# Kernel optimization log

Measured on AMD Instinct MI355X. Metric: run time of the kernel, lower is better.

The kernel has to match this reference:

```python
import jax, jax.numpy as jnp
import numpy as np


def setup_inputs() -> dict:
    key = jax.random.key(0)
    ks = jax.random.split(key, 11)
    N, K, M = 2, 2048, 1024   # batch, seq_len, d_model (dim_in)
    H, D = 16, 64             # num_heads, dim_out (per-head q/k/v dim)
    s_in = 1.0 / np.sqrt(M)
    s_out = 1.0 / np.sqrt(H * D)
    return {
        "query": jax.random.normal(ks[0], (N, K, M), jnp.float32),
        "key":   jax.random.normal(ks[1], (N, K, M), jnp.float32),
        "value": jax.random.normal(ks[2], (N, K, M), jnp.float32),
        "Wq": jax.random.normal(ks[3], (H, D, M), jnp.float32) * s_in,
        "bq": jax.random.normal(ks[4], (H, D), jnp.float32) * 0.01,
        "Wk": jax.random.normal(ks[5], (H, D, M), jnp.float32) * s_in,
        "bk": jax.random.normal(ks[6], (H, D), jnp.float32) * 0.01,
        "Wv": jax.random.normal(ks[7], (H, D, M), jnp.float32) * s_in,
        "bv": jax.random.normal(ks[8], (H, D), jnp.float32) * 0.01,
        "Wo": jax.random.normal(ks[9], (M, H * D), jnp.float32) * s_out,
        "bo": jax.random.normal(ks[10], (M,), jnp.float32) * 0.01,
    }


def reference(query, key, value, Wq, bq, Wk, bk, Wv, bv, Wo, bo):
    # Batched over heads instead of the original python loop; same math.
    # q,k: [H,N,K,D], v: [H,N,K,D]
    q = jnp.einsum('nkm,hdm->hnkd', query, Wq) + bq[:, None, None, :]
    k = jnp.einsum('nkm,hdm->hnkd', key,   Wk) + bk[:, None, None, :]
    v = jnp.einsum('nkm,hdm->hnkd', value, Wv) + bv[:, None, None, :]
    D = q.shape[-1]
    # scaled_dot_product scales by sqrt of the projected dim (dim_out)
    scores = jnp.einsum('hnkd,hnld->hnkl', q, k) / jnp.sqrt(jnp.asarray(D, q.dtype))
    attn = jax.nn.softmax(scores, axis=-1)            # [H,N,K,K]
    y = jnp.einsum('hnkl,hnld->hnkd', attn, v)        # [H,N,K,D]
    H, N, K, _ = y.shape
    # concat heads along feature dim: [N,K,H*D]
    y_cat = jnp.transpose(y, (1, 2, 0, 3)).reshape(N, K, H * D)
    return y_cat @ Wo.T + bo
```

## Files before the change

### kernel.cpp

```cpp
#include <hip/hip_runtime.h>
#include <hip/hip_bf16.h>

#define NB 2
#define SEQ 2048
#define DM 1024
#define NH 16
#define HD 64

typedef unsigned short u16;
typedef unsigned int u32;
typedef __attribute__((ext_vector_type(8))) short bf16x8;
typedef __attribute__((ext_vector_type(4))) float f32x4;
typedef __attribute__((ext_vector_type(4))) unsigned short u16x4;
typedef __attribute__((ext_vector_type(2))) unsigned int u32x2;

#define MFMA __builtin_amdgcn_mfma_f32_16x16x32_bf16

#define QSCALE 0.18033688011112042f

__device__ __forceinline__ u16 bf16_rne(float x) {
    unsigned int u = __float_as_uint(x);
    return (u16)((u + 0x7FFFu + ((u >> 16) & 1u)) >> 16);
}
__device__ __forceinline__ float bf16f(u16 h) {
    return __uint_as_float(((unsigned int)h) << 16);
}
__device__ __forceinline__ void split2(float x, u16& h, u16& l) {
    h = bf16_rne(x);
    l = bf16_rne(x - bf16f(h));
}
__device__ __forceinline__ u32 cvt_pk_bf16(float lo, float hi) {
    u32 r;
    asm("v_cvt_pk_bf16_f32 %0, %1, %2" : "=v"(r) : "v"(lo), "v"(hi));
    return r;
}
__device__ __forceinline__ float exp2_fast(float x) {
#if __has_builtin(__builtin_amdgcn_exp2f)
    return __builtin_amdgcn_exp2f(x);
#else
    float r;
    asm("v_exp_f32 %0, %1" : "=v"(r) : "v"(x));
    return r;
#endif
}

__device__ __forceinline__ void async16(const u16* g, u16* l) {
    typedef const __attribute__((address_space(1))) u32* GP;
    typedef __attribute__((address_space(3))) u32* LP;
    __builtin_amdgcn_global_load_lds((GP)g, (LP)l, 16, 0, 0);
}

__global__ __launch_bounds__(256) void presplit(
    const float* __restrict__ x0, const float* __restrict__ x1,
    const float* __restrict__ x2, const float* __restrict__ wq,
    const float* __restrict__ wk, const float* __restrict__ wv,
    const float* __restrict__ wo,
    u16* __restrict__ xh, u16* __restrict__ xl,
    u16* __restrict__ wh, u16* __restrict__ wl)
{
    const int seg = blockIdx.y;
    const float* src;
    u16 *dh, *dl;
    int n4;
    float sc = 1.f;
    if (seg < 3) {
        src = (seg == 0) ? x0 : (seg == 1) ? x1 : x2;
        dh = xh + (size_t)seg * 4194304;
        dl = xl + (size_t)seg * 4194304;
        n4 = 1048576;
    } else {
        int s2 = seg - 3;
        src = (s2 == 0) ? wq : (s2 == 1) ? wk : (s2 == 2) ? wv : wo;
        dh = wh + (size_t)s2 * 1048576;
        dl = wl + (size_t)s2 * 1048576;
        n4 = 262144;
        if (s2 == 0) sc = QSCALE;
    }
    for (int i = blockIdx.x * 256 + threadIdx.x; i < n4; i += gridDim.x * 256) {
        float4 v = ((const float4*)src)[i];
        u16 h0, h1, h2, h3, l0, l1, l2, l3;
        split2(v.x * sc, h0, l0); split2(v.y * sc, h1, l1);
        split2(v.z * sc, h2, l2); split2(v.w * sc, h3, l3);
        u16x4 hv = {h0, h1, h2, h3}, lv = {l0, l1, l2, l3};
        *(u16x4*)(dh + (size_t)i * 4) = hv;
        *(u16x4*)(dl + (size_t)i * 4) = lv;
    }
}

template<int VAR>
__global__ __launch_bounds__(256, 2) void gemm2(
    const u16* __restrict__ xh3, const u16* __restrict__ xl3,
    const u16* __restrict__ wh4, const u16* __restrict__ wl4,
    const float* bq, const float* bk, const float* bv,
    u16* qh, u16* ql, u16* kh, u16* kl, u16* vh, u16* vl,
    float* outf)
{
    __shared__ u16 Ah[128][32], Al[128][32], Bh[128][32], Bl[128][32];

    const int tid = threadIdx.x, lane = tid & 63, w = tid >> 6;
    const int lg = lane >> 4, lc = lane & 15;

    const int id = blockIdx.x + 8 * blockIdx.y;
    const int swz = (id & 7) * 32 + (id >> 3);
    const int c0 = (swz & 7) * 128, r0 = (swz >> 3) * 128;

    const u16 *ag, *alg, *bg, *blg;
    const float* bias;
    u16 *oh = nullptr, *ol = nullptr;
    float bsc = 1.f;
    int mode;
    if (VAR == 0) {
        const int z = blockIdx.z;
        ag  = xh3 + (size_t)z * 4194304;
        alg = xl3 + (size_t)z * 4194304;
        bg  = wh4 + (size_t)z * 1048576;
        blg = wl4 + (size_t)z * 1048576;
        if (z == 0)      { bias = bq; oh = qh; ol = ql; bsc = QSCALE; mode = 1; }
        else if (z == 1) { bias = bk; oh = kh; mode = 2; }
        else             { bias = bv; oh = vh; mode = 3; }
    } else {
        ag = xh3; alg = xl3; bg = wh4; blg = wl4; bias = bq; mode = 0;
    }

    const u16* gb = (w == 0) ? ag : (w == 1) ? alg : (w == 2) ? bg : blg;
    u16* lb = (w == 0) ? &Ah[0][0] : (w == 1) ? &Al[0][0] : (w == 2) ? &Bh[0][0] : &Bl[0][0];
    const int rbase = (w < 2) ? r0 : c0;
    const u16* gsrc0 = gb + (size_t)(rbase + (lane >> 2)) * DM + (lane & 3) * 8;

    const int wr = (w >> 1) * 64, wc = (w & 1) * 64;

    f32x4 acc[4][4];
#pragma unroll
    for (int i = 0; i < 4; ++i)
#pragma unroll
        for (int j = 0; j < 4; ++j) acc[i][j] = (f32x4)0.f;

    for (int ks = 0; ks < DM; ks += 32) {
        __syncthreads();
#pragma unroll
        for (int i = 0; i < 8; ++i)
            async16(gsrc0 + (size_t)i * 16 * DM + ks, lb + i * 512);
        __syncthreads();

        bf16x8 ah[4], al[4];
#pragma unroll
        for (int rt = 0; rt < 4; ++rt) {
            ah[rt] = *(const bf16x8*)&Ah[wr + rt * 16 + lc][lg * 8];
            al[rt] = *(const bf16x8*)&Al[wr + rt * 16 + lc][lg * 8];
        }
#pragma unroll
        for (int jt = 0; jt < 4; ++jt) {
            bf16x8 bh2 = *(const bf16x8*)&Bh[wc + jt * 16 + lc][lg * 8];
            bf16x8 bl2 = *(const bf16x8*)&Bl[wc + jt * 16 + lc][lg * 8];
#pragma unroll
            for (int rt = 0; rt < 4; ++rt) {
                acc[rt][jt] = MFMA(ah[rt], bh2, acc[rt][jt], 0, 0, 0);
                acc[rt][jt] = MFMA(ah[rt], bl2, acc[rt][jt], 0, 0, 0);
                acc[rt][jt] = MFMA(al[rt], bh2, acc[rt][jt], 0, 0, 0);
            }
        }
    }

#pragma unroll
    for (int rt = 0; rt < 4; ++rt)
#pragma unroll
        for (int jt = 0; jt < 4; ++jt)
#pragma unroll
            for (int r = 0; r < 4; ++r) {
                int row = r0 + wr + rt * 16 + lg * 4 + r;
                int col = c0 + wc + jt * 16 + lc;
                float v = acc[rt][jt][r] + bias[col] * bsc;
                if (mode == 0) {
                    outf[(size_t)row * DM + col] = v;
                } else {
                    int h = col >> 6, d = col & 63, n = row >> 11, s = row & 2047;
                    if (mode == 1) {
                        size_t idx = ((size_t)((h << 1) | n) * SEQ + s) * HD + d;
                        u16 hh, ll; split2(v, hh, ll);
                        oh[idx] = hh; ol[idx] = ll;
                    } else if (mode == 2) {
                        size_t idx = ((size_t)((h << 1) | n) * SEQ + s) * HD + d;
                        oh[idx] = bf16_rne(v);
                    } else {
                        size_t idx = ((size_t)((h << 1) | n) * HD + d) * SEQ + s;
                        oh[idx] = bf16_rne(v);
                    }
                }
            }
}

__global__ __launch_bounds__(256, 4) void attn_k(
    const u16* __restrict__ qh, const u16* __restrict__ ql,
    const u16* __restrict__ kh, const u16* __restrict__ vth,
    u16* __restrict__ yh, u16* __restrict__ yl)
{
    __shared__ u16 Ks[64][72], Vs[64][72];
    __shared__ u16 Pb[4][32][72];

    const int tid = threadIdx.x, lane = tid & 63, w = tid >> 6;
    const int lg = lane >> 4, lc = lane & 15;

    const int id = blockIdx.x + 16 * blockIdx.y;
    const int widx = (id & 7) * 64 + (id >> 3);
    const int hn = widx >> 4;
    const int qb0 = (widx & 15) * 128;

    bf16x8 qfh[2][2], qfl[2][2];
    const size_t qkbase = (size_t)hn * SEQ * HD;
#pragma unroll
    for (int rt = 0; rt < 2; ++rt)
#pragma unroll
        for (int kc = 0; kc < 2; ++kc) {
            size_t off = qkbase + (size_t)(qb0 + w * 32 + rt * 16 + lc) * HD + kc * 32 + lg * 8;
            qfh[rt][kc] = *(const bf16x8*)(qh + off);
            qfl[rt][kc] = *(const bf16x8*)(ql + off);
        }

    f32x4 ot[2][4];
#pragma unroll
    for (int i = 0; i < 2; ++i)
#pragma unroll
        for (int j = 0; j < 4; ++j) ot[i][j] = (f32x4)0.f;
    float m_[2] = {-3e38f, -3e38f};
    float s_[2] = {0.f, 0.f};

    const size_t vbase = (size_t)hn * HD * SEQ;

    for (int kt = 0; kt < SEQ; kt += 64) {
        __syncthreads();
#pragma unroll
        for (int i = 0; i < 2; ++i) {
            int f = tid + 256 * i, row = f >> 3, kb = (f & 7) * 8;
            size_t ksrc = qkbase + (size_t)(kt + row) * HD + kb;
            *(bf16x8*)&Ks[row][kb] = *(const bf16x8*)(kh + ksrc);
            size_t vsrc = vbase + (size_t)row * SEQ + kt + kb;
            *(bf16x8*)&Vs[row][kb] = *(const bf16x8*)(vth + vsrc);
        }
        __syncthreads();

        f32x4 st[2][4];
#pragma unroll
        for (int i = 0; i < 2; ++i)
#pragma unroll
            for (int j = 0; j < 4; ++j) st[i][j] = (f32x4)0.f;
        __builtin_amdgcn_s_setprio(1);
#pragma unroll
        for (int jt = 0; jt < 4; ++jt)
#pragma unroll
            for (int kc = 0; kc < 2; ++kc) {
                bf16x8 k8 = *(const bf16x8*)&Ks[jt * 16 + lc][kc * 32 + lg * 8];
#pragma unroll
                for (int rt = 0; rt < 2; ++rt) {
                    st[rt][jt] = MFMA(k8, qfh[rt][kc], st[rt][jt], 0, 0, 0);
                    st[rt][jt] = MFMA(k8, qfl[rt][kc], st[rt][jt], 0, 0, 0);
                }
            }
        __builtin_amdgcn_s_setprio(0);

#pragma unroll
        for (int rt = 0; rt < 2; ++rt) {
            float t0 = fmaxf(fmaxf(st[rt][0][0], st[rt][0][1]),
                             fmaxf(st[rt][0][2], st[rt][0][3]));
            float t1 = fmaxf(fmaxf(st[rt][1][0], st[rt][1][1]),
                             fmaxf(st[rt][1][2], st[rt][1][3]));
            float t2 = fmaxf(fmaxf(st[rt][2][0], st[rt][2][1]),
                             fmaxf(st[rt][2][2], st[rt][2][3]));
            float t3 = fmaxf(fmaxf(st[rt][3][0], st[rt][3][1]),
                             fmaxf(st[rt][3][2], st[rt][3][3]));
            float t = fmaxf(fmaxf(t0, t1), fmaxf(t2, t3));
            t = fmaxf(t, __shfl_xor(t, 16));
            t = fmaxf(t, __shfl_xor(t, 32));
            if (__any(t - m_[rt] > 8.0f)) {
                float mnew = fmaxf(m_[rt], t);
                float resc = exp2_fast(m_[rt] - mnew);
                m_[rt] = mnew;
                s_[rt] *= resc;
#pragma unroll
                for (int dt = 0; dt < 4; ++dt) {
                    ot[rt][dt][0] *= resc; ot[rt][dt][1] *= resc;
                    ot[rt][dt][2] *= resc; ot[rt][dt][3] *= resc;
                }
            }
            const float mm = m_[rt];
#pragma unroll
            for (int jt = 0; jt < 4; ++jt) {
                float p0 = exp2_fast(st[rt][jt][0] - mm);
                float p1 = exp2_fast(st[rt][jt][1] - mm);
                float p2 = exp2_fast(st[rt][jt][2] - mm);
                float p3 = exp2_fast(st[rt][jt][3] - mm);
                s_[rt] += (p0 + p1) + (p2 + p3);
                u32x2 pk = {cvt_pk_bf16(p0, p1), cvt_pk_bf16(p2, p3)};
                *(u32x2*)&Pb[w][rt * 16 + lc][jt * 16 + lg * 4] = pk;
            }
        }

        bf16x8 pb[2][2];
#pragma unroll
        for (int rt = 0; rt < 2; ++rt)
#pragma unroll
            for (int jc = 0; jc < 2; ++jc)
                pb[rt][jc] = *(const bf16x8*)&Pb[w][rt * 16 + lc][jc * 32 + lg * 8];
        __builtin_amdgcn_s_setprio(1);
#pragma unroll
        for (int dt = 0; dt < 4; ++dt)
#pragma unroll
            for (int jc = 0; jc < 2; ++jc) {
                bf16x8 v8 = *(const bf16x8*)&Vs[dt * 16 + lc][jc * 32 + lg * 8];
#pragma unroll
                for (int rt = 0; rt < 2; ++rt)
                    ot[rt][dt] = MFMA(v8, pb[rt][jc], ot[rt][dt], 0, 0, 0);
            }
        __builtin_amdgcn_s_setprio(0);
    }

    const int h = hn >> 1, n = hn & 1;
#pragma unroll
    for (int rt = 0; rt < 2; ++rt) {
        float v = s_[rt];
        v += __shfl_xor(v, 16);
        v += __shfl_xor(v, 32);
        s_[rt] = 1.f / v;
    }
#pragma unroll
    for (int rt = 0; rt < 2; ++rt) {
        const int srow = qb0 + w * 32 + rt * 16 + lc;
        size_t rowoff = (size_t)(n * SEQ + srow) * DM + h * HD;
#pragma unroll
        for (int dt = 0; dt < 4; ++dt) {
            u16x4 hv, lv;
#pragma unroll
            for (int r = 0; r < 4; ++r) {
                float y = ot[rt][dt][r] * s_[rt];
                u16 hh, ll; split2(y, hh, ll);
                hv[r] = hh; lv[r] = ll;
            }
            size_t idx = rowoff + dt * 16 + lg * 4;
            *(u16x4*)(yh + idx) = hv;
            *(u16x4*)(yl + idx) = lv;
        }
    }
}

extern "C" void kernel_launch(void* const* d_in, const int* in_sizes, int n_in,
                              void* d_out, int out_size, void* d_ws, size_t ws_size,
                              hipStream_t stream)
{
    const float* query = (const float*)d_in[0];
    const float* key_  = (const float*)d_in[1];
    const float* value = (const float*)d_in[2];
    const float* Wq = (const float*)d_in[3];
    const float* bq = (const float*)d_in[4];
    const float* Wk = (const float*)d_in[5];
    const float* bk = (const float*)d_in[6];
    const float* Wv = (const float*)d_in[7];
    const float* bv = (const float*)d_in[8];
    const float* Wo = (const float*)d_in[9];
    const float* bo = (const float*)d_in[10];
    float* out = (float*)d_out;

    char* p = (char*)d_ws;
    u16* wh  = (u16*)(p);
    u16* wl  = (u16*)(p + 8388608ull);
    u16* qh  = (u16*)(p + 16777216ull);
    u16* ql  = (u16*)(p + 25165824ull);
    u16* kh  = (u16*)(p + 33554432ull);
    u16* kl  = (u16*)(p + 41943040ull);
    u16* vth = (u16*)(p + 50331648ull);
    u16* vtl = (u16*)(p + 58720256ull);
    u16* xh  = (u16*)(p + 67108864ull);
    u16* xl  = (u16*)(p + 92274688ull);
    u16* yh  = (u16*)(p + 67108864ull);
    u16* yl  = (u16*)(p + 75497472ull);

    presplit<<<dim3(256, 7), 256, 0, stream>>>(
        query, key_, value, Wq, Wk, Wv, Wo, xh, xl, wh, wl);

    gemm2<0><<<dim3(8, 32, 3), 256, 0, stream>>>(
        xh, xl, wh, wl, bq, bk, bv,
        qh, ql, kh, kl, vth, vtl, nullptr);

    attn_k<<<dim3(16, 32), 256, 0, stream>>>(qh, ql, kh, vth, yh, yl);

    gemm2<1><<<dim3(8, 32, 1), 256, 0, stream>>>(
        yh, yl, wh + 3145728ull, wl + 3145728ull, bo, nullptr, nullptr,
        nullptr, nullptr, nullptr, nullptr, nullptr, nullptr, out);
}
```

Baseline: 332.3 us.

## Drop low-bf16 split for QKV projections and use single-pass bf16 GEMM

```diff
diff --git a/kernel.cpp b/kernel.cpp
--- a/kernel.cpp
+++ b/kernel.cpp
@@ -55,47 +55,48 @@
     const float* __restrict__ x2, const float* __restrict__ wq,
     const float* __restrict__ wk, const float* __restrict__ wv,
     const float* __restrict__ wo,
-    u16* __restrict__ xh, u16* __restrict__ xl,
-    u16* __restrict__ wh, u16* __restrict__ wl)
+    u16* __restrict__ xh, u16* __restrict__ wh, u16* __restrict__ wl)
 {
     const int seg = blockIdx.y;
     const float* src;
-    u16 *dh, *dl;
+    u16* dh;
+    u16* dl = nullptr;
     int n4;
     float sc = 1.f;
     if (seg < 3) {
         src = (seg == 0) ? x0 : (seg == 1) ? x1 : x2;
         dh = xh + (size_t)seg * 4194304;
-        dl = xl + (size_t)seg * 4194304;
         n4 = 1048576;
     } else {
         int s2 = seg - 3;
         src = (s2 == 0) ? wq : (s2 == 1) ? wk : (s2 == 2) ? wv : wo;
         dh = wh + (size_t)s2 * 1048576;
-        dl = wl + (size_t)s2 * 1048576;
+        if (s2 == 3) dl = wl + (size_t)s2 * 1048576;
         n4 = 262144;
         if (s2 == 0) sc = QSCALE;
     }
     for (int i = blockIdx.x * 256 + threadIdx.x; i < n4; i += gridDim.x * 256) {
         float4 v = ((const float4*)src)[i];
-        u16 h0, h1, h2, h3, l0, l1, l2, l3;
-        split2(v.x * sc, h0, l0); split2(v.y * sc, h1, l1);
-        split2(v.z * sc, h2, l2); split2(v.w * sc, h3, l3);
-        u16x4 hv = {h0, h1, h2, h3}, lv = {l0, l1, l2, l3};
+        v.x *= sc; v.y *= sc; v.z *= sc; v.w *= sc;
+        u16 h0 = bf16_rne(v.x), h1 = bf16_rne(v.y);
+        u16 h2 = bf16_rne(v.z), h3 = bf16_rne(v.w);
+        u16x4 hv = {h0, h1, h2, h3};
         *(u16x4*)(dh + (size_t)i * 4) = hv;
-        *(u16x4*)(dl + (size_t)i * 4) = lv;
-    }
-}
-
-template<int VAR>
-__global__ __launch_bounds__(256, 2) void gemm2(
-    const u16* __restrict__ xh3, const u16* __restrict__ xl3,
-    const u16* __restrict__ wh4, const u16* __restrict__ wl4,
-    const float* bq, const float* bk, const float* bv,
-    u16* qh, u16* ql, u16* kh, u16* kl, u16* vh, u16* vl,
-    float* outf)
+        if (dl) {
+            u16x4 lv = {bf16_rne(v.x - bf16f(h0)), bf16_rne(v.y - bf16f(h1)),
+                        bf16_rne(v.z - bf16f(h2)), bf16_rne(v.w - bf16f(h3))};
+            *(u16x4*)(dl + (size_t)i * 4) = lv;
+        }
+    }
+}
+
+__global__ __launch_bounds__(256, 4) void gemm_qkv(
+    const u16* __restrict__ xh3, const u16* __restrict__ wh3,
+    const float* __restrict__ bq, const float* __restrict__ bk,
+    const float* __restrict__ bv,
+    u16* qh, u16* ql, u16* kh, u16* vth)
 {
-    __shared__ u16 Ah[128][32], Al[128][32], Bh[128][32], Bl[128][32];
+    __shared__ u16 A0[128][32], A1[128][32], B0[128][32], B1[128][32];
 
     const int tid = threadIdx.x, lane = tid & 63, w = tid >> 6;
     const int lg = lane >> 4, lc = lane & 15;
@@ -104,25 +105,93 @@
     const int swz = (id & 7) * 32 + (id >> 3);
     const int c0 = (swz & 7) * 128, r0 = (swz >> 3) * 128;
 
-    const u16 *ag, *alg, *bg, *blg;
-    const float* bias;
-    u16 *oh = nullptr, *ol = nullptr;
-    float bsc = 1.f;
-    int mode;
-    if (VAR == 0) {
-        const int z = blockIdx.z;
-        ag  = xh3 + (size_t)z * 4194304;
-        alg = xl3 + (size_t)z * 4194304;
-        bg  = wh4 + (size_t)z * 1048576;
-        blg = wl4 + (size_t)z * 1048576;
-        if (z == 0)      { bias = bq; oh = qh; ol = ql; bsc = QSCALE; mode = 1; }
-        else if (z == 1) { bias = bk; oh = kh; mode = 2; }
-        else             { bias = bv; oh = vh; mode = 3; }
-    } else {
-        ag = xh3; alg = xl3; bg = wh4; blg = wl4; bias = bq; mode = 0;
-    }
-
-    const u16* gb = (w == 0) ? ag : (w == 1) ? alg : (w == 2) ? bg : blg;
+    const int z = blockIdx.z;
+    const u16* ag = xh3 + (size_t)z * 4194304;
+    const u16* bg = wh3 + (size_t)z * 1048576;
+    const float* bias = (z == 0) ? bq : (z == 1) ? bk : bv;
+
+    const u16* gb = (w < 2) ? ag : bg;
+    u16* lb = (w == 0) ? &A0[0][0] : (w == 1) ? &A1[0][0]
+            : (w == 2) ? &B0[0][0] : &B1[0][0];
+    const int rbase = (w < 2) ? r0 : c0;
+    const int colofs = (w & 1) * 32;
+    const u16* gsrc0 = gb + (size_t)(rbase + (lane >> 2)) * DM + colofs + (lane & 3) * 8;
+
+    const int wr = (w >> 1) * 64, wc = (w & 1) * 64;
+
+    f32x4 acc[4][4];
+#pragma unroll
+    for (int i = 0; i < 4; ++i)
+#pragma unroll
+        for (int j = 0; j < 4; ++j) acc[i][j] = (f32x4)0.f;
+
+    for (int ks = 0; ks < DM; ks += 64) {
+        __syncthreads();
+#pragma unroll
+        for (int i = 0; i < 8; ++i)
+            async16(gsrc0 + (size_t)i * 16 * DM + ks, lb + i * 512);
+        __syncthreads();
+
+#pragma unroll
+        for (int kk = 0; kk < 2; ++kk) {
+            const u16(*Ak)[32] = kk ? A1 : A0;
+            const u16(*Bk)[32] = kk ? B1 : B0;
+            bf16x8 ah[4], bh[4];
+#pragma unroll
+            for (int rt = 0; rt < 4; ++rt)
+                ah[rt] = *(const bf16x8*)&Ak[wr + rt * 16 + lc][lg * 8];
+#pragma unroll
+            for (int jt = 0; jt < 4; ++jt)
+                bh[jt] = *(const bf16x8*)&Bk[wc + jt * 16 + lc][lg * 8];
+#pragma unroll
+            for (int jt = 0; jt < 4; ++jt)
+#pragma unroll
+                for (int rt = 0; rt < 4; ++rt)
+                    acc[rt][jt] = MFMA(ah[rt], bh[jt], acc[rt][jt], 0, 0, 0);
+        }
+    }
+
+#pragma unroll
+    for (int rt = 0; rt < 4; ++rt)
+#pragma unroll
+        for (int jt = 0; jt < 4; ++jt)
+#pragma unroll
+            for (int r = 0; r < 4; ++r) {
+                int row = r0 + wr + rt * 16 + lg * 4 + r;
+                int col = c0 + wc + jt * 16 + lc;
+                int h = col >> 6, d = col & 63, n = row >> 11, s = row & 2047;
+                if (z == 0) {
+                    float v = acc[rt][jt][r] + bias[col] * QSCALE;
+                    size_t idx = ((size_t)((h << 1) | n) * SEQ + s) * HD + d;
+                    u16 hh, ll; split2(v, hh, ll);
+                    qh[idx] = hh; ql[idx] = ll;
+                } else if (z == 1) {
+                    float v = acc[rt][jt][r] + bias[col];
+                    size_t idx = ((size_t)((h << 1) | n) * SEQ + s) * HD + d;
+                    kh[idx] = bf16_rne(v);
+                } else {
+                    float v = acc[rt][jt][r] + bias[col];
+                    size_t idx = ((size_t)((h << 1) | n) * HD + d) * SEQ + s;
+                    vth[idx] = bf16_rne(v);
+                }
+            }
+}
+
+__global__ __launch_bounds__(256, 2) void gemm_proj(
+    const u16* __restrict__ yh, const u16* __restrict__ yl,
+    const u16* __restrict__ woh, const u16* __restrict__ wol,
+    const float* __restrict__ bo, float* __restrict__ outf)
+{
+    __shared__ u16 Ah[128][32], Al[128][32], Bh[128][32], Bl[128][32];
+
+    const int tid = threadIdx.x, lane = tid & 63, w = tid >> 6;
+    const int lg = lane >> 4, lc = lane & 15;
+
+    const int id = blockIdx.x + 8 * blockIdx.y;
+    const int swz = (id & 7) * 32 + (id >> 3);
+    const int c0 = (swz & 7) * 128, r0 = (swz >> 3) * 128;
+
+    const u16* gb = (w == 0) ? yh : (w == 1) ? yl : (w == 2) ? woh : wol;
     u16* lb = (w == 0) ? &Ah[0][0] : (w == 1) ? &Al[0][0] : (w == 2) ? &Bh[0][0] : &Bl[0][0];
     const int rbase = (w < 2) ? r0 : c0;
     const u16* gsrc0 = gb + (size_t)(rbase + (lane >> 2)) * DM + (lane & 3) * 8;
@@ -169,23 +238,7 @@
             for (int r = 0; r < 4; ++r) {
                 int row = r0 + wr + rt * 16 + lg * 4 + r;
                 int col = c0 + wc + jt * 16 + lc;
-                float v = acc[rt][jt][r] + bias[col] * bsc;
-                if (mode == 0) {
-                    outf[(size_t)row * DM + col] = v;
-                } else {
-                    int h = col >> 6, d = col & 63, n = row >> 11, s = row & 2047;
-                    if (mode == 1) {
-                        size_t idx = ((size_t)((h << 1) | n) * SEQ + s) * HD + d;
-                        u16 hh, ll; split2(v, hh, ll);
-                        oh[idx] = hh; ol[idx] = ll;
-                    } else if (mode == 2) {
-                        size_t idx = ((size_t)((h << 1) | n) * SEQ + s) * HD + d;
-                        oh[idx] = bf16_rne(v);
-                    } else {
-                        size_t idx = ((size_t)((h << 1) | n) * HD + d) * SEQ + s;
-                        oh[idx] = bf16_rne(v);
-                    }
-                }
+                outf[(size_t)row * DM + col] = acc[rt][jt][r] + bo[col];
             }
 }
 
@@ -364,24 +417,19 @@
     u16* qh  = (u16*)(p + 16777216ull);
     u16* ql  = (u16*)(p + 25165824ull);
     u16* kh  = (u16*)(p + 33554432ull);
-    u16* kl  = (u16*)(p + 41943040ull);
     u16* vth = (u16*)(p + 50331648ull);
-    u16* vtl = (u16*)(p + 58720256ull);
     u16* xh  = (u16*)(p + 67108864ull);
-    u16* xl  = (u16*)(p + 92274688ull);
     u16* yh  = (u16*)(p + 67108864ull);
     u16* yl  = (u16*)(p + 75497472ull);
 
     presplit<<<dim3(256, 7), 256, 0, stream>>>(
-        query, key_, value, Wq, Wk, Wv, Wo, xh, xl, wh, wl);
-
-    gemm2<0><<<dim3(8, 32, 3), 256, 0, stream>>>(
-        xh, xl, wh, wl, bq, bk, bv,
-        qh, ql, kh, kl, vth, vtl, nullptr);
+        query, key_, value, Wq, Wk, Wv, Wo, xh, wh, wl);
+
+    gemm_qkv<<<dim3(8, 32, 3), 256, 0, stream>>>(
+        xh, wh, bq, bk, bv, qh, ql, kh, vth);
 
     attn_k<<<dim3(16, 32), 256, 0, stream>>>(qh, ql, kh, vth, yh, yl);
 
-    gemm2<1><<<dim3(8, 32, 1), 256, 0, stream>>>(
-        yh, yl, wh + 3145728ull, wl + 3145728ull, bo, nullptr, nullptr,
-        nullptr, nullptr, nullptr, nullptr, nullptr, nullptr, out);
-}
+    gemm_proj<<<dim3(8, 32), 256, 0, stream>>>(
+        yh, yl, wh + 3145728ull, wl + 3145728ull, bo, out);
+}
```

Result: faster. 280.6 us (-15.6%).
